# Kernel tuning notes

Hardware: AMD Instinct MI355X
Metric: run time of the kernel (lower is better)

Reference implementation:

```python
import jax, jax.numpy as jnp
import numpy as np

S = 256          # spatial coordinate range per axis
B = 2            # batch size
R = S + 2        # packing radix (padded so +-1 kernel offsets stay in range)
C = 64           # feature channels


def _pack(xyz, b):
    """Collision-free integer packing of (x,y,z,batch) -> int64 key.
    Faithful stand-in for torchsparse F.sphash (an injective hash of 4D coords)."""
    xyz = xyz.astype(jnp.int64) + 1  # shift so offset -1 maps to >= 0
    b = b.astype(jnp.int64)
    return ((b * R + xyz[:, 0]) * R + xyz[:, 1]) * R + xyz[:, 2]


def _offsets():
    # get_kernel_offsets(3, stride=input_stride=1, dilation=1): odd kernel -> z-major order
    r = np.arange(-1, 2)
    return np.array([[x, y, z] for z in r for y in r for x in r], dtype=np.int32)  # [27, 3]


def setup_inputs() -> dict:
    rng = np.random.default_rng(0)
    N0 = 1_200_000
    xyz = rng.integers(0, S, size=(N0, 3))
    bat = rng.integers(0, B, size=(N0, 1))
    coords = np.unique(np.concatenate([xyz, bat], axis=1), axis=0).astype(np.int32)  # [N,4]
    # spdownsample(coords, stride=2): floor to stride grid, unique rows
    dc = coords.copy()
    dc[:, :3] = dc[:, :3] // 2 * 2
    down_coords = np.unique(dc, axis=0).astype(np.int32)  # [M,4]
    key = jax.random.key(0)
    feats = jax.random.normal(key, (coords.shape[0], C), dtype=jnp.float32)
    return {
        "feats": feats,
        "coords": jnp.asarray(coords),
        "down_coords": jnp.asarray(down_coords),
    }


def reference(feats, coords, down_coords):
    N = feats.shape[0]
    # references = sphash(coords); build sorted key table for hash queries
    refs = _pack(coords[:, :3], coords[:, 3])
    order = jnp.argsort(refs)
    refs_sorted = refs[order]
    neg = jnp.asarray(-jnp.inf, feats.dtype)
    out = jnp.full((down_coords.shape[0], feats.shape[1]), neg, feats.dtype)
    # queries = sphash(down_coords, offsets); results = sphashquery; voxel_scatter_max
    # (output row of each nbmap entry is the query row, so scatter-max reduces to a
    #  per-row running maximum over the 27 fixed kernel offsets)
    for off in _offsets():
        q = _pack(down_coords[:, :3] + jnp.asarray(off), down_coords[:, 3])
        pos = jnp.clip(jnp.searchsorted(refs_sorted, q), 0, N - 1)
        match = refs_sorted[pos] == q            # [M] valid-neighbor mask (result != -1)
        src = order[pos]                          # [M] input voxel index per query
        out = jnp.maximum(out, jnp.where(match[:, None], feats[src], neg))
    # rows with no neighbor (cannot happen for stride-2 floor downsample) -> 0
    return jnp.where(jnp.isinf(out), jnp.asarray(0.0, feats.dtype), out)
```

## Files before the change

kernel.cpp:

```cpp
#include <hip/hip_runtime.h>
#include <cstdint>
#include <cstddef>

#define RADIX 258
#define EMPTY_ENTRY 0xFFFFFFFFFFFFFFFFULL
#define MAP_DIM 128
#define MAP_SLOTS (2 * MAP_DIM * MAP_DIM * MAP_DIM)
#define NB_STRIDE 32

typedef float f32x4 __attribute__((ext_vector_type(4)));


__global__ __launch_bounds__(256) void build_map_kernel(
    const int* __restrict__ down, int M, unsigned* __restrict__ map)
{
    int j = blockIdx.x * blockDim.x + threadIdx.x;
    if (j >= M) return;
    const int4 c = ((const int4*)down)[j];
    unsigned idx = (((unsigned)(c.w * MAP_DIM + (c.x >> 1)) * MAP_DIM)
                    + (unsigned)(c.y >> 1)) * MAP_DIM + (unsigned)(c.z >> 1);
    map[idx] = (unsigned)j;
}

__global__ __launch_bounds__(256) void scatter_kernel(
    const int* __restrict__ coords, int N,
    const unsigned* __restrict__ map,
    unsigned* __restrict__ cnt, unsigned* __restrict__ nbmap)
{
    int i = blockIdx.x * blockDim.x + threadIdx.x;
    if (i >= N) return;
    const int4 c = ((const int4*)coords)[i];
    int qx[2], qy[2], qz[2];
    int nx = 1, ny = 1, nz = 1;
    if (c.x & 1) { qx[0] = (c.x - 1) >> 1; if (c.x + 1 <= 254) qx[nx++] = (c.x + 1) >> 1; }
    else         { qx[0] = c.x >> 1; }
    if (c.y & 1) { qy[0] = (c.y - 1) >> 1; if (c.y + 1 <= 254) qy[ny++] = (c.y + 1) >> 1; }
    else         { qy[0] = c.y >> 1; }
    if (c.z & 1) { qz[0] = (c.z - 1) >> 1; if (c.z + 1 <= 254) qz[nz++] = (c.z + 1) >> 1; }
    else         { qz[0] = c.z >> 1; }
    unsigned bbase = (unsigned)(c.w * MAP_DIM);
    for (int ix = 0; ix < nx; ++ix) {
        unsigned xb = (bbase + (unsigned)qx[ix]) * MAP_DIM;
        for (int iy = 0; iy < ny; ++iy) {
            unsigned yb = (xb + (unsigned)qy[iy]) * MAP_DIM;
            for (int iz = 0; iz < nz; ++iz) {
                unsigned qi = map[yb + (unsigned)qz[iz]];
                if (qi != 0xFFFFFFFFu) {
                    unsigned pos = atomicAdd(&cnt[qi], 1u);
                    nbmap[(size_t)qi * NB_STRIDE + 1 + pos] = (unsigned)i;
                }
            }
        }
    }
}

__global__ __launch_bounds__(256) void gather_kernel(
    const float* __restrict__ feats,
    const unsigned* __restrict__ cnt,
    const unsigned* __restrict__ nbmap,
    float* __restrict__ out, int M, int nblk)
{
    int bid = blockIdx.x;
    int q8 = nblk >> 3, r8 = nblk & 7;
    int xcd = bid & 7, orig = bid >> 3;
    int swz = (xcd < r8 ? xcd * (q8 + 1) : r8 * (q8 + 1) + (xcd - r8) * q8) + orig;

    int lane = threadIdx.x & 63;
    int g  = lane >> 4;
    int j  = lane & 15;
    int gb = g << 4;
    int wv   = swz * 4 + (int)(threadIdx.x >> 6);
    int totW = nblk * 4;
    int nq   = (M + 3) >> 2;

    const f32x4* f4 = (const f32x4*)feats;

    int q = wv;
    unsigned u = 0;
    if (q < nq) {
        int row = q * 4 + g;
        if (row < M)
            u = (j == 0) ? __builtin_nontemporal_load(cnt + row)
                         : __builtin_nontemporal_load(nbmap + (size_t)row * NB_STRIDE + j);
    }
    for (; q < nq; q += totW) {
        int row = q * 4 + g;
        unsigned un = 0;
        int qn = q + totW;
        if (qn < nq) {
            int rown = qn * 4 + g;
            if (rown < M)
                un = (j == 0) ? __builtin_nontemporal_load(cnt + rown)
                              : __builtin_nontemporal_load(nbmap + (size_t)rown * NB_STRIDE + j);
        }

        int c = __shfl((int)u, gb);
        f32x4 acc = {-INFINITY, -INFINITY, -INFINITY, -INFINITY};
        for (int r4 = 0; r4 < c; r4 += 4) {
#pragma unroll
            for (int k = 0; k < 4; ++k) {
                int h = r4 + k;
                if (h < c) {
                    int s = (h < 15) ? __shfl((int)u, gb + 1 + h)
                                     : (int)nbmap[(size_t)row * NB_STRIDE + 1 + h];
                    f32x4 v = f4[(size_t)s * 16 + j];
                    acc.x = fmaxf(acc.x, v.x);
                    acc.y = fmaxf(acc.y, v.y);
                    acc.z = fmaxf(acc.z, v.z);
                    acc.w = fmaxf(acc.w, v.w);
                }
            }
        }
        if (row < M) {
            if (c == 0) acc = (f32x4){0.f, 0.f, 0.f, 0.f};
            __builtin_nontemporal_store(acc, (f32x4*)out + (size_t)row * 16 + j);
        }
        u = un;
    }
}


__global__ __launch_bounds__(256) void build_hash_kernel(
    const int* __restrict__ coords, int N,
    unsigned long long* __restrict__ tab, unsigned tmask, int tshift)
{
    int i = blockIdx.x * blockDim.x + threadIdx.x;
    if (i >= N) return;
    int x = coords[i * 4 + 0];
    int y = coords[i * 4 + 1];
    int z = coords[i * 4 + 2];
    int b = coords[i * 4 + 3];
    unsigned key = ((unsigned)(b * RADIX + x + 1) * RADIX + (unsigned)(y + 1)) * RADIX
                   + (unsigned)(z + 1);
    unsigned long long entry = ((unsigned long long)key << 32) | (unsigned)i;
    unsigned slot = (key * 2654435761u) >> tshift;
    while (true) {
        unsigned long long prev = atomicCAS(&tab[slot], EMPTY_ENTRY, entry);
        if (prev == EMPTY_ENTRY) break;
        slot = (slot + 1) & tmask;
    }
}

__global__ __launch_bounds__(256) void pool_kernel(
    const float* __restrict__ feats,
    const int* __restrict__ down, int M,
    const unsigned long long* __restrict__ tab, unsigned tmask, int tshift,
    float* __restrict__ out)
{
    int wave = (int)((blockIdx.x * blockDim.x + threadIdx.x) >> 6);
    int lane = threadIdx.x & 63;
    if (wave >= M) return;

    const int* dc = down + (size_t)wave * 4;
    int dx = dc[0], dy = dc[1], dz = dc[2], db = dc[3];
    unsigned base = ((unsigned)(db * RADIX + dx + 1) * RADIX + (unsigned)(dy + 1)) * RADIX
                    + (unsigned)(dz + 1);

    int src = -1;
    if (lane < 27) {
        int ox = lane % 3 - 1;
        int oy = (lane / 3) % 3 - 1;
        int oz = lane / 9 - 1;
        int delta = ox * (RADIX * RADIX) + oy * RADIX + oz;
        unsigned key = (unsigned)((int)base + delta);
        unsigned slot = (key * 2654435761u) >> tshift;
        while (true) {
            unsigned long long e = tab[slot];
            if (e == EMPTY_ENTRY) break;
            if ((unsigned)(e >> 32) == key) { src = (int)(unsigned)e; break; }
            slot = (slot + 1) & tmask;
        }
    }
    unsigned long long mask = __ballot(src >= 0);
    float acc = -INFINITY;
    while (mask) {
        int bit = __ffsll(mask) - 1;
        int s = __shfl(src, bit);
        acc = fmaxf(acc, feats[(size_t)s * 64 + lane]);
        mask &= mask - 1;
    }
    out[(size_t)wave * 64 + lane] = isinf(acc) ? 0.0f : acc;
}


extern "C" void kernel_launch(void* const* d_in, const int* in_sizes, int n_in,
                              void* d_out, int out_size, void* d_ws, size_t ws_size,
                              hipStream_t stream)
{
    const float* feats  = (const float*)d_in[0];
    const int*   coords = (const int*)d_in[1];
    const int*   down   = (const int*)d_in[2];
    float*       out    = (float*)d_out;

    int N = in_sizes[1] / 4;
    int M = in_sizes[2] / 4;

    size_t map_bytes = (size_t)MAP_SLOTS * 4;
    size_t cnt_bytes = ((size_t)M * 4 + 127) & ~(size_t)127;
    size_t nb_bytes  = (size_t)M * NB_STRIDE * 4;
    size_t need = map_bytes + cnt_bytes + nb_bytes;

    if (ws_size >= need) {
        unsigned* map   = (unsigned*)d_ws;
        unsigned* cnt   = (unsigned*)((char*)d_ws + map_bytes);
        unsigned* nbmap = (unsigned*)((char*)d_ws + map_bytes + cnt_bytes);

        hipMemsetAsync(map, 0xFF, map_bytes, stream);
        hipMemsetAsync(cnt, 0x00, (size_t)M * 4, stream);

        build_map_kernel<<<(M + 255) / 256, 256, 0, stream>>>(down, M, map);
        scatter_kernel<<<(N + 255) / 256, 256, 0, stream>>>(coords, N, map, cnt, nbmap);

        int nq = (M + 3) / 4;
        int nblk = (nq + 3) / 4;
        if (nblk > 2048) nblk = 2048;
        gather_kernel<<<nblk, 256, 0, stream>>>(feats, cnt, nbmap, out, M, nblk);
    } else {
        int logT = 22;
        while (logT > 19 && ((size_t)8u << logT) > ws_size) logT--;
        unsigned T = 1u << logT;
        unsigned tmask = T - 1u;
        int tshift = 32 - logT;
        unsigned long long* tab = (unsigned long long*)d_ws;
        hipMemsetAsync(tab, 0xFF, (size_t)T * 8, stream);
        build_hash_kernel<<<(N + 255) / 256, 256, 0, stream>>>(coords, N, tab, tmask, tshift);
        pool_kernel<<<(M * 64 + 255) / 256, 256, 0, stream>>>(
            feats, down, M, tab, tmask, tshift, out);
    }
}
```

Before: 223.4 us.

## Compact neighbor map to 64B rows and software-pipeline feature gathers across iterations

Neighbor lists are stored as 16-word rows, with overflow entries beyond 15 moved to a separate extension array, which halves the nbmap footprint and write traffic. The gather kernel now prefetches neighbor lists two iterations ahead and issues the first four feature loads of the next row before reducing the current one, so load latency overlaps with compute. This raises register pressure and adds a branch in the scatter kernel for the overflow path.

```diff
diff --git a/kernel.cpp b/kernel.cpp
--- a/kernel.cpp
+++ b/kernel.cpp
@@ -6,9 +6,12 @@
 #define EMPTY_ENTRY 0xFFFFFFFFFFFFFFFFULL
 #define MAP_DIM 128
 #define MAP_SLOTS (2 * MAP_DIM * MAP_DIM * MAP_DIM)
-#define NB_STRIDE 32
+#define NB_WORDS 16
+#define EXT_WORDS 12
 
 typedef float f32x4 __attribute__((ext_vector_type(4)));
+
+#define NEGINF4 ((f32x4){-INFINITY, -INFINITY, -INFINITY, -INFINITY})
 
 
 __global__ __launch_bounds__(256) void build_map_kernel(
@@ -25,7 +28,8 @@
 __global__ __launch_bounds__(256) void scatter_kernel(
     const int* __restrict__ coords, int N,
     const unsigned* __restrict__ map,
-    unsigned* __restrict__ cnt, unsigned* __restrict__ nbmap)
+    unsigned* __restrict__ cnt, unsigned* __restrict__ nbmap,
+    unsigned* __restrict__ ext)
 {
     int i = blockIdx.x * blockDim.x + threadIdx.x;
     if (i >= N) return;
@@ -47,7 +51,10 @@
                 unsigned qi = map[yb + (unsigned)qz[iz]];
                 if (qi != 0xFFFFFFFFu) {
                     unsigned pos = atomicAdd(&cnt[qi], 1u);
-                    nbmap[(size_t)qi * NB_STRIDE + 1 + pos] = (unsigned)i;
+                    if (pos < 15)
+                        nbmap[(size_t)qi * NB_WORDS + pos] = (unsigned)i;
+                    else
+                        ext[(size_t)qi * EXT_WORDS + (pos - 15)] = (unsigned)i;
                 }
             }
         }
@@ -58,6 +65,7 @@
     const float* __restrict__ feats,
     const unsigned* __restrict__ cnt,
     const unsigned* __restrict__ nbmap,
+    const unsigned* __restrict__ ext,
     float* __restrict__ out, int M, int nblk)
 {
     int bid = blockIdx.x;
@@ -75,47 +83,76 @@
 
     const f32x4* f4 = (const f32x4*)feats;
 
+    auto load_line = [&](int qq) -> unsigned {
+        unsigned v = 0;
+        int rw = qq * 4 + g;
+        if (qq < nq && rw < M)
+            v = (j == 0) ? __builtin_nontemporal_load(cnt + rw)
+                         : __builtin_nontemporal_load(nbmap + (size_t)rw * NB_WORDS + (j - 1));
+        return v;
+    };
+
     int q = wv;
-    unsigned u = 0;
-    if (q < nq) {
-        int row = q * 4 + g;
-        if (row < M)
-            u = (j == 0) ? __builtin_nontemporal_load(cnt + row)
-                         : __builtin_nontemporal_load(nbmap + (size_t)row * NB_STRIDE + j);
-    }
-    for (; q < nq; q += totW) {
-        int row = q * 4 + g;
-        unsigned un = 0;
+    unsigned uA = load_line(q);
+    unsigned uB = load_line(q + totW);
+    int cC = __shfl((int)uA, gb);
+    f32x4 v0 = NEGINF4, v1 = NEGINF4, v2 = NEGINF4, v3 = NEGINF4;
+    {
+        int s0 = __shfl((int)uA, gb + 1);
+        int s1 = __shfl((int)uA, gb + 2);
+        int s2 = __shfl((int)uA, gb + 3);
+        int s3 = __shfl((int)uA, gb + 4);
+        if (0 < cC) v0 = f4[(size_t)s0 * 16 + j];
+        if (1 < cC) v1 = f4[(size_t)s1 * 16 + j];
+        if (2 < cC) v2 = f4[(size_t)s2 * 16 + j];
+        if (3 < cC) v3 = f4[(size_t)s3 * 16 + j];
+    }
+
+    for (; q < nq; ) {
         int qn = q + totW;
-        if (qn < nq) {
-            int rown = qn * 4 + g;
-            if (rown < M)
-                un = (j == 0) ? __builtin_nontemporal_load(cnt + rown)
-                              : __builtin_nontemporal_load(nbmap + (size_t)rown * NB_STRIDE + j);
-        }
-
-        int c = __shfl((int)u, gb);
-        f32x4 acc = {-INFINITY, -INFINITY, -INFINITY, -INFINITY};
-        for (int r4 = 0; r4 < c; r4 += 4) {
-#pragma unroll
-            for (int k = 0; k < 4; ++k) {
-                int h = r4 + k;
-                if (h < c) {
-                    int s = (h < 15) ? __shfl((int)u, gb + 1 + h)
-                                     : (int)nbmap[(size_t)row * NB_STRIDE + 1 + h];
-                    f32x4 v = f4[(size_t)s * 16 + j];
-                    acc.x = fmaxf(acc.x, v.x);
-                    acc.y = fmaxf(acc.y, v.y);
-                    acc.z = fmaxf(acc.z, v.z);
-                    acc.w = fmaxf(acc.w, v.w);
-                }
+        unsigned uC = load_line(qn + totW);
+
+        int cN = __shfl((int)uB, gb);
+        f32x4 w0 = NEGINF4, w1 = NEGINF4, w2 = NEGINF4, w3 = NEGINF4;
+        {
+            int s0 = __shfl((int)uB, gb + 1);
+            int s1 = __shfl((int)uB, gb + 2);
+            int s2 = __shfl((int)uB, gb + 3);
+            int s3 = __shfl((int)uB, gb + 4);
+            if (0 < cN) w0 = f4[(size_t)s0 * 16 + j];
+            if (1 < cN) w1 = f4[(size_t)s1 * 16 + j];
+            if (2 < cN) w2 = f4[(size_t)s2 * 16 + j];
+            if (3 < cN) w3 = f4[(size_t)s3 * 16 + j];
+        }
+
+        {
+            int row = q * 4 + g;
+            f32x4 acc = NEGINF4;
+            if (0 < cC) { acc.x = fmaxf(acc.x, v0.x); acc.y = fmaxf(acc.y, v0.y);
+                          acc.z = fmaxf(acc.z, v0.z); acc.w = fmaxf(acc.w, v0.w); }
+            if (1 < cC) { acc.x = fmaxf(acc.x, v1.x); acc.y = fmaxf(acc.y, v1.y);
+                          acc.z = fmaxf(acc.z, v1.z); acc.w = fmaxf(acc.w, v1.w); }
+            if (2 < cC) { acc.x = fmaxf(acc.x, v2.x); acc.y = fmaxf(acc.y, v2.y);
+                          acc.z = fmaxf(acc.z, v2.z); acc.w = fmaxf(acc.w, v2.w); }
+            if (3 < cC) { acc.x = fmaxf(acc.x, v3.x); acc.y = fmaxf(acc.y, v3.y);
+                          acc.z = fmaxf(acc.z, v3.z); acc.w = fmaxf(acc.w, v3.w); }
+            for (int h = 4; h < cC; ++h) {
+                int s = (h < 15) ? __shfl((int)uA, gb + 1 + h)
+                                 : (int)ext[(size_t)row * EXT_WORDS + (h - 15)];
+                f32x4 vv = f4[(size_t)s * 16 + j];
+                acc.x = fmaxf(acc.x, vv.x); acc.y = fmaxf(acc.y, vv.y);
+                acc.z = fmaxf(acc.z, vv.z); acc.w = fmaxf(acc.w, vv.w);
             }
-        }
-        if (row < M) {
-            if (c == 0) acc = (f32x4){0.f, 0.f, 0.f, 0.f};
-            __builtin_nontemporal_store(acc, (f32x4*)out + (size_t)row * 16 + j);
-        }
-        u = un;
+            if (row < M) {
+                if (cC == 0) acc = (f32x4){0.f, 0.f, 0.f, 0.f};
+                __builtin_nontemporal_store(acc, (f32x4*)out + (size_t)row * 16 + j);
+            }
+        }
+
+        uA = uB; uB = uC;
+        v0 = w0; v1 = w1; v2 = w2; v3 = w3;
+        cC = cN;
+        q = qn;
     }
 }
 
@@ -197,24 +234,27 @@
 
     size_t map_bytes = (size_t)MAP_SLOTS * 4;
     size_t cnt_bytes = ((size_t)M * 4 + 127) & ~(size_t)127;
-    size_t nb_bytes  = (size_t)M * NB_STRIDE * 4;
-    size_t need = map_bytes + cnt_bytes + nb_bytes;
+    size_t nb_bytes  = (size_t)M * NB_WORDS * 4;
+    size_t ext_bytes = (size_t)M * EXT_WORDS * 4;
+    size_t need = map_bytes + cnt_bytes + nb_bytes + ext_bytes;
 
     if (ws_size >= need) {
-        unsigned* map   = (unsigned*)d_ws;
-        unsigned* cnt   = (unsigned*)((char*)d_ws + map_bytes);
-        unsigned* nbmap = (unsigned*)((char*)d_ws + map_bytes + cnt_bytes);
+        char* p = (char*)d_ws;
+        unsigned* map   = (unsigned*)p;                 p += map_bytes;
+        unsigned* cnt   = (unsigned*)p;                 p += cnt_bytes;
+        unsigned* nbmap = (unsigned*)p;                 p += nb_bytes;
+        unsigned* ext   = (unsigned*)p;
 
         hipMemsetAsync(map, 0xFF, map_bytes, stream);
         hipMemsetAsync(cnt, 0x00, (size_t)M * 4, stream);
 
         build_map_kernel<<<(M + 255) / 256, 256, 0, stream>>>(down, M, map);
-        scatter_kernel<<<(N + 255) / 256, 256, 0, stream>>>(coords, N, map, cnt, nbmap);
+        scatter_kernel<<<(N + 255) / 256, 256, 0, stream>>>(coords, N, map, cnt, nbmap, ext);
 
         int nq = (M + 3) / 4;
         int nblk = (nq + 3) / 4;
         if (nblk > 2048) nblk = 2048;
-        gather_kernel<<<nblk, 256, 0, stream>>>(feats, cnt, nbmap, out, M, nblk);
+        gather_kernel<<<nblk, 256, 0, stream>>>(feats, cnt, nbmap, ext, out, M, nblk);
     } else {
         int logT = 22;
         while (logT > 19 && ((size_t)8u << logT) > ws_size) logT--;
```

Result: faster. 206.4 us (-7.6%).

## Compact neighbor map to 8 words and software-pipeline feature gathers across rows

Applied to the files above, without the earlier changes.

Shrinks each output row's neighbor list from 32 words to 8 inline words, with an overflow array for rarer larger counts. The gather kernel now uses a multi-stage pipeline: it loads metadata several iterations ahead and issues the first four feature loads two rows ahead, so memory latency overlaps with the max reduction. The aim is to cut neighbor-map traffic and hide gather latency. The cost is more registers, redundant loads for rows with fewer than four neighbors, and a slower path for rows with more than four.

```diff
diff --git a/kernel.cpp b/kernel.cpp
--- a/kernel.cpp
+++ b/kernel.cpp
@@ -6,7 +6,8 @@
 #define EMPTY_ENTRY 0xFFFFFFFFFFFFFFFFULL
 #define MAP_DIM 128
 #define MAP_SLOTS (2 * MAP_DIM * MAP_DIM * MAP_DIM)
-#define NB_STRIDE 32
+#define NB_WORDS 8
+#define EXT_WORDS 19
 
 typedef float f32x4 __attribute__((ext_vector_type(4)));
 
@@ -25,7 +26,8 @@
 __global__ __launch_bounds__(256) void scatter_kernel(
     const int* __restrict__ coords, int N,
     const unsigned* __restrict__ map,
-    unsigned* __restrict__ cnt, unsigned* __restrict__ nbmap)
+    unsigned* __restrict__ cnt, unsigned* __restrict__ nbmap,
+    unsigned* __restrict__ ext)
 {
     int i = blockIdx.x * blockDim.x + threadIdx.x;
     if (i >= N) return;
@@ -47,7 +49,10 @@
                 unsigned qi = map[yb + (unsigned)qz[iz]];
                 if (qi != 0xFFFFFFFFu) {
                     unsigned pos = atomicAdd(&cnt[qi], 1u);
-                    nbmap[(size_t)qi * NB_STRIDE + 1 + pos] = (unsigned)i;
+                    if (pos < NB_WORDS)
+                        nbmap[(size_t)qi * NB_WORDS + pos] = (unsigned)i;
+                    else
+                        ext[(size_t)qi * EXT_WORDS + (pos - NB_WORDS)] = (unsigned)i;
                 }
             }
         }
@@ -58,6 +63,7 @@
     const float* __restrict__ feats,
     const unsigned* __restrict__ cnt,
     const unsigned* __restrict__ nbmap,
+    const unsigned* __restrict__ ext,
     float* __restrict__ out, int M, int nblk)
 {
     int bid = blockIdx.x;
@@ -68,54 +74,91 @@
     int lane = threadIdx.x & 63;
     int g  = lane >> 4;
     int j  = lane & 15;
-    int gb = g << 4;
-    int wv   = swz * 4 + (int)(threadIdx.x >> 6);
-    int totW = nblk * 4;
-    int nq   = (M + 3) >> 2;
-
-    const f32x4* f4 = (const f32x4*)feats;
+    int wv = swz * 4 + (int)(threadIdx.x >> 6);
+    int T  = nblk * 4;
+    int nq = (M + 3) >> 2;
+
+    const f32x4* f4  = (const f32x4*)feats;
+    const int4*  nb4 = (const int4*)nbmap;
+
+    auto rowof = [&](int qq) -> int {
+        int qc = qq < nq ? qq : nq - 1;
+        int r = qc * 4 + g;
+        return r < M ? r : M - 1;
+    };
+    auto load_meta = [&](int qq, int& c, int4& idx) {
+        int r = rowof(qq);
+        c   = (int)cnt[r];
+        idx = nb4[(size_t)r * 2];
+    };
+    auto issue_feats = [&](int c, int4 idx,
+                           f32x4& w0, f32x4& w1, f32x4& w2, f32x4& w3) {
+        int s0 = c > 0 ? idx.x : 0;
+        int s1 = c > 1 ? idx.y : s0;
+        int s2 = c > 2 ? idx.z : s0;
+        int s3 = c > 3 ? idx.w : s0;
+        w0 = f4[(size_t)s0 * 16 + j];
+        w1 = f4[(size_t)s1 * 16 + j];
+        w2 = f4[(size_t)s2 * 16 + j];
+        w3 = f4[(size_t)s3 * 16 + j];
+    };
 
     int q = wv;
-    unsigned u = 0;
-    if (q < nq) {
-        int row = q * 4 + g;
-        if (row < M)
-            u = (j == 0) ? __builtin_nontemporal_load(cnt + row)
-                         : __builtin_nontemporal_load(nbmap + (size_t)row * NB_STRIDE + j);
-    }
-    for (; q < nq; q += totW) {
-        int row = q * 4 + g;
-        unsigned un = 0;
-        int qn = q + totW;
-        if (qn < nq) {
-            int rown = qn * 4 + g;
-            if (rown < M)
-                un = (j == 0) ? __builtin_nontemporal_load(cnt + rown)
-                              : __builtin_nontemporal_load(nbmap + (size_t)rown * NB_STRIDE + j);
-        }
-
-        int c = __shfl((int)u, gb);
-        f32x4 acc = {-INFINITY, -INFINITY, -INFINITY, -INFINITY};
-        for (int r4 = 0; r4 < c; r4 += 4) {
-#pragma unroll
-            for (int k = 0; k < 4; ++k) {
-                int h = r4 + k;
-                if (h < c) {
-                    int s = (h < 15) ? __shfl((int)u, gb + 1 + h)
-                                     : (int)nbmap[(size_t)row * NB_STRIDE + 1 + h];
-                    f32x4 v = f4[(size_t)s * 16 + j];
-                    acc.x = fmaxf(acc.x, v.x);
-                    acc.y = fmaxf(acc.y, v.y);
-                    acc.z = fmaxf(acc.z, v.z);
-                    acc.w = fmaxf(acc.w, v.w);
+    int cA; int4 iA; load_meta(q,         cA, iA);
+    int cB; int4 iB; load_meta(q + T,     cB, iB);
+    int c2; int4 i2; load_meta(q + 2 * T, c2, i2);
+    int c3; int4 i3; load_meta(q + 3 * T, c3, i3);
+
+    f32x4 v0, v1, v2, v3, p0, p1, p2, p3, w0, w1, w2, w3;
+    issue_feats(cA, iA, v0, v1, v2, v3);
+    issue_feats(cB, iB, p0, p1, p2, p3);
+    int c0 = cA, c1 = cB;
+
+    for (; q < nq; q += T) {
+        int cN; int4 iN; load_meta(q + 4 * T, cN, iN);
+        issue_feats(c2, i2, w0, w1, w2, w3);
+        int cPush = c2;
+
+        {
+            int row = rowof(q);
+            f32x4 acc;
+            acc.x = fmaxf(fmaxf(v0.x, v1.x), fmaxf(v2.x, v3.x));
+            acc.y = fmaxf(fmaxf(v0.y, v1.y), fmaxf(v2.y, v3.y));
+            acc.z = fmaxf(fmaxf(v0.z, v1.z), fmaxf(v2.z, v3.z));
+            acc.w = fmaxf(fmaxf(v0.w, v1.w), fmaxf(v2.w, v3.w));
+            int c = c0;
+            if (c > 4) {
+                int4 e = nb4[(size_t)row * 2 + 1];
+                int cc = c < 8 ? c : 8;
+                f32x4 t;
+                if (cc > 4) { t = f4[(size_t)e.x * 16 + j];
+                    acc.x = fmaxf(acc.x, t.x); acc.y = fmaxf(acc.y, t.y);
+                    acc.z = fmaxf(acc.z, t.z); acc.w = fmaxf(acc.w, t.w); }
+                if (cc > 5) { t = f4[(size_t)e.y * 16 + j];
+                    acc.x = fmaxf(acc.x, t.x); acc.y = fmaxf(acc.y, t.y);
+                    acc.z = fmaxf(acc.z, t.z); acc.w = fmaxf(acc.w, t.w); }
+                if (cc > 6) { t = f4[(size_t)e.z * 16 + j];
+                    acc.x = fmaxf(acc.x, t.x); acc.y = fmaxf(acc.y, t.y);
+                    acc.z = fmaxf(acc.z, t.z); acc.w = fmaxf(acc.w, t.w); }
+                if (cc > 7) { t = f4[(size_t)e.w * 16 + j];
+                    acc.x = fmaxf(acc.x, t.x); acc.y = fmaxf(acc.y, t.y);
+                    acc.z = fmaxf(acc.z, t.z); acc.w = fmaxf(acc.w, t.w); }
+                for (int h = 8; h < c; ++h) {
+                    int s = (int)ext[(size_t)row * EXT_WORDS + (h - 8)];
+                    t = f4[(size_t)s * 16 + j];
+                    acc.x = fmaxf(acc.x, t.x); acc.y = fmaxf(acc.y, t.y);
+                    acc.z = fmaxf(acc.z, t.z); acc.w = fmaxf(acc.w, t.w);
                 }
             }
-        }
-        if (row < M) {
             if (c == 0) acc = (f32x4){0.f, 0.f, 0.f, 0.f};
             __builtin_nontemporal_store(acc, (f32x4*)out + (size_t)row * 16 + j);
         }
-        u = un;
+
+        v0 = p0; v1 = p1; v2 = p2; v3 = p3;
+        p0 = w0; p1 = w1; p2 = w2; p3 = w3;
+        c0 = c1; c1 = cPush;
+        c2 = c3; i2 = i3;
+        c3 = cN; i3 = iN;
     }
 }
 
@@ -197,24 +240,27 @@
 
     size_t map_bytes = (size_t)MAP_SLOTS * 4;
     size_t cnt_bytes = ((size_t)M * 4 + 127) & ~(size_t)127;
-    size_t nb_bytes  = (size_t)M * NB_STRIDE * 4;
-    size_t need = map_bytes + cnt_bytes + nb_bytes;
+    size_t nb_bytes  = (size_t)(M + 4) * NB_WORDS * 4;
+    size_t ext_bytes = (size_t)M * EXT_WORDS * 4;
+    size_t need = map_bytes + cnt_bytes + nb_bytes + ext_bytes;
 
     if (ws_size >= need) {
-        unsigned* map   = (unsigned*)d_ws;
-        unsigned* cnt   = (unsigned*)((char*)d_ws + map_bytes);
-        unsigned* nbmap = (unsigned*)((char*)d_ws + map_bytes + cnt_bytes);
+        char* p = (char*)d_ws;
+        unsigned* map   = (unsigned*)p;                 p += map_bytes;
+        unsigned* cnt   = (unsigned*)p;                 p += cnt_bytes;
+        unsigned* nbmap = (unsigned*)p;                 p += nb_bytes;
+        unsigned* ext   = (unsigned*)p;
 
         hipMemsetAsync(map, 0xFF, map_bytes, stream);
         hipMemsetAsync(cnt, 0x00, (size_t)M * 4, stream);
 
         build_map_kernel<<<(M + 255) / 256, 256, 0, stream>>>(down, M, map);
-        scatter_kernel<<<(N + 255) / 256, 256, 0, stream>>>(coords, N, map, cnt, nbmap);
+        scatter_kernel<<<(N + 255) / 256, 256, 0, stream>>>(coords, N, map, cnt, nbmap, ext);
 
         int nq = (M + 3) / 4;
         int nblk = (nq + 3) / 4;
         if (nblk > 2048) nblk = 2048;
-        gather_kernel<<<nblk, 256, 0, stream>>>(feats, cnt, nbmap, out, M, nblk);
+        gather_kernel<<<nblk, 256, 0, stream>>>(feats, cnt, nbmap, ext, out, M, nblk);
     } else {
         int logT = 22;
         while (logT > 19 && ((size_t)8u << logT) > ws_size) logT--;
```

Measured after the change: 207.3 us. -7.2%, faster.
